# Optimization experiments

Hardware: AMD Instinct MI355X
Metric: run time of the kernel (lower is better)

## Reference

```python
import jax, jax.numpy as jnp
import numpy as np

D_MODEL, D_K, D_V = 1024, 64, 128
NUM_HEAD = D_MODEL // D_V  # 8


def setup_inputs() -> dict:
    key = jax.random.key(0)
    ks = jax.random.split(key, 6)
    B, SQ, SKV = 4, 2048, 2048
    return {
        "encoder_output": jax.random.normal(ks[0], (B, SKV, D_MODEL), jnp.float32),
        "pre_output": jax.random.normal(ks[1], (B, SQ, D_MODEL), jnp.float32),
        "Wq": jax.random.normal(ks[2], (D_MODEL, D_K * NUM_HEAD), jnp.float32) * 0.02,
        "Wk": jax.random.normal(ks[3], (D_MODEL, D_K * NUM_HEAD), jnp.float32) * 0.02,
        "Wv": jax.random.normal(ks[4], (D_MODEL, D_MODEL), jnp.float32) * 0.02,
        "Wo": jax.random.normal(ks[5], (D_MODEL, D_MODEL), jnp.float32) * 0.02,
    }


def reference(encoder_output, pre_output, Wq, Wk, Wv, Wo):
    B, SQ, _ = pre_output.shape
    SKV = encoder_output.shape[1]
    # projections (Linear, bias=False)
    q = pre_output @ Wq          # [B, SQ, H*d_k]
    k = encoder_output @ Wk      # [B, SKV, H*d_k]
    v = encoder_output @ Wv      # [B, SKV, H*d_v] (= d_model)
    # per-head contiguous slices == reshape into head dim
    q = q.reshape(B, SQ, NUM_HEAD, D_K)
    k = k.reshape(B, SKV, NUM_HEAD, D_K)
    v = v.reshape(B, SKV, NUM_HEAD, D_V)
    scale = 1.0 / np.sqrt(D_K).astype(np.float32)
    scores = jnp.einsum("bqhd,bkhd->bhqk", q, k) * scale  # [B,H,SQ,SKV]
    attn = jax.nn.softmax(scores, axis=-1)
    out = jnp.einsum("bhqk,bkhd->bqhd", attn, v)           # [B,SQ,H,d_v]
    out = out.reshape(B, SQ, NUM_HEAD * D_V)               # concat heads
    return out @ Wo
```

## Files before the change

kernel.cpp:

```cpp
#include <hip/hip_runtime.h>
#include <math.h>

#define D_MODEL 1024
#define DK 64
#define DV 128
#define NH 8
#define BB 4
#define SQL 2048
#define SKV 2048

typedef __bf16 bf16x8 __attribute__((ext_vector_type(8)));
typedef float f32x4 __attribute__((ext_vector_type(4)));

#if __has_builtin(__builtin_amdgcn_exp2f)
#define EXP2(x) __builtin_amdgcn_exp2f(x)
#else
#define EXP2(x) exp2f(x)
#endif

__device__ __forceinline__ ushort f2bf(float f) {
  unsigned u = __float_as_uint(f);
  u += 0x7FFFu + ((u >> 16) & 1u);
  return (ushort)(u >> 16);
}

#define GLDS16(g, l)                                                       \
  __builtin_amdgcn_global_load_lds(                                        \
      (const __attribute__((address_space(1))) unsigned int*)(g),          \
      (__attribute__((address_space(3))) unsigned int*)(l), 16, 0, 0)

__global__ __launch_bounds__(256) void cvt2_kernel(
    const float* __restrict__ s0, const float* __restrict__ s1,
    ushort* __restrict__ d0, ushort* __restrict__ d1, int n4) {
  const float* src = blockIdx.z ? s1 : s0;
  ushort* dst = blockIdx.z ? d1 : d0;
  int i = blockIdx.x * 256 + threadIdx.x;
  if (i >= n4) return;
  float4 v = ((const float4*)src)[i];
  ushort4 o;
  o.x = f2bf(v.x); o.y = f2bf(v.y); o.z = f2bf(v.z); o.w = f2bf(v.w);
  ((ushort4*)dst)[i] = o;
}

__global__ __launch_bounds__(256) void cvt_t4_kernel(
    const float* __restrict__ W0, const float* __restrict__ W1,
    const float* __restrict__ W2, const float* __restrict__ W3,
    ushort* __restrict__ T0, ushort* __restrict__ T1, ushort* __restrict__ T2,
    ushort* __restrict__ T3) {
  __shared__ ushort T[32][34];
  const int z = blockIdx.z;
  const int C = (z < 2) ? 512 : 1024;
  const int c0 = blockIdx.y * 32;
  if (c0 >= C) return;
  const float* W = (z == 0) ? W0 : (z == 1) ? W1 : (z == 2) ? W2 : W3;
  ushort* Wt = (z == 0) ? T0 : (z == 1) ? T1 : (z == 2) ? T2 : T3;
  const int R = 1024;
  const int r0 = blockIdx.x * 32;
  const int tx = threadIdx.x, ty = threadIdx.y;
#pragma unroll
  for (int i = 0; i < 4; ++i) {
    const int rr = ty + i * 8;
    T[rr][tx] = f2bf(W[(size_t)(r0 + rr) * C + c0 + tx]);
  }
  __syncthreads();
#pragma unroll
  for (int i = 0; i < 4; ++i) {
    const int rr = ty + i * 8;
    Wt[(size_t)(c0 + rr) * R + r0 + tx] = T[tx][rr];
  }
}

__global__ __launch_bounds__(256) void vtrans_kernel(
    const ushort* __restrict__ vb, ushort* __restrict__ vt) {
  __shared__ ushort T[32][34];
  const int s0 = blockIdx.x * 32;
  const int d0 = blockIdx.y * 32;
  const int bh = blockIdx.z;
  const int b = bh >> 3, h = bh & 7;
  const int tx = threadIdx.x, ty = threadIdx.y;
#pragma unroll
  for (int i = 0; i < 4; ++i) {
    const int rr = ty + i * 8;
    T[rr][tx] = vb[(size_t)(b * SKV + s0 + rr) * (NH * DV) + h * DV + d0 + tx];
  }
  __syncthreads();
#pragma unroll
  for (int i = 0; i < 4; ++i) {
    const int rr = ty + i * 8;
    vt[(size_t)bh * DV * SKV + (size_t)(d0 + rr) * SKV + s0 + tx] = T[tx][rr];
  }
}

template <typename OUT>
__device__ __forceinline__ void gemm_tile_core(ushort (*As)[32],
                                               ushort (*Bs)[32],
                                               const ushort* At,
                                               const ushort* Bt, OUT* Ct,
                                               int ldc, float osc, int K) {
  const int t = threadIdx.x;
  const int w = t >> 6, lane = t & 63;
  const int wm = (w >> 1) * 64, wn = (w & 1) * 64;
  const int lr = lane & 15, quad = lane >> 4;

  const int r0 = t >> 2;
  const int lb = (t & 3) ^ ((r0 >> 1) & 3);
  const ushort* gA0 = At + (size_t)r0 * K + lb * 8;
  const ushort* gA1 = At + (size_t)(r0 + 64) * K + lb * 8;
  const ushort* gB0 = Bt + (size_t)r0 * K + lb * 8;
  const ushort* gB1 = Bt + (size_t)(r0 + 64) * K + lb * 8;
  ushort* dA0 = (ushort*)As + t * 8;
  ushort* dA1 = (ushort*)As + t * 8 + 2048;
  ushort* dB0 = (ushort*)Bs + t * 8;
  ushort* dB1 = (ushort*)Bs + t * 8 + 2048;

  const int sw = (quad ^ ((lr >> 1) & 3)) * 8;

  f32x4 acc[4][4];
#pragma unroll
  for (int i = 0; i < 4; ++i)
#pragma unroll
    for (int j = 0; j < 4; ++j) acc[i][j] = (f32x4){0.f, 0.f, 0.f, 0.f};

  for (int k0 = 0; k0 < K; k0 += 32) {
    __syncthreads();
    GLDS16(gA0 + k0, dA0);
    GLDS16(gA1 + k0, dA1);
    GLDS16(gB0 + k0, dB0);
    GLDS16(gB1 + k0, dB1);
    __syncthreads();
    bf16x8 fa[4], fb[4];
#pragma unroll
    for (int i = 0; i < 4; ++i) fa[i] = *(const bf16x8*)&As[wm + i * 16 + lr][sw];
#pragma unroll
    for (int j = 0; j < 4; ++j) fb[j] = *(const bf16x8*)&Bs[wn + j * 16 + lr][sw];
#pragma unroll
    for (int i = 0; i < 4; ++i)
#pragma unroll
      for (int j = 0; j < 4; ++j)
        acc[i][j] = __builtin_amdgcn_mfma_f32_16x16x32_bf16(fa[i], fb[j],
                                                            acc[i][j], 0, 0, 0);
  }

#pragma unroll
  for (int i = 0; i < 4; ++i)
#pragma unroll
    for (int j = 0; j < 4; ++j)
#pragma unroll
      for (int r = 0; r < 4; ++r) {
        const int row = wm + i * 16 + quad * 4 + r;
        const int col = wn + j * 16 + lr;
        const float val = acc[i][j][r] * osc;
        if constexpr (sizeof(OUT) == 4)
          ((float*)Ct)[(size_t)row * ldc + col] = val;
        else
          ((ushort*)Ct)[(size_t)row * ldc + col] = f2bf(val);
      }
}

__global__ __launch_bounds__(256) void gemm_qkv_kernel(
    const ushort* __restrict__ preb, const ushort* __restrict__ encb,
    const ushort* __restrict__ WqkvT, ushort* __restrict__ qb,
    ushort* __restrict__ kb, ushort* __restrict__ vb, float qsc) {
  __shared__ ushort As[128][32];
  __shared__ ushort Bs[128][32];
  const int n0 = blockIdx.x * 128, m0 = blockIdx.y * 128;
  const int K = D_MODEL;
  const ushort* A;
  ushort* C;
  int ldc, ncol;
  float osc = 1.f;
  if (n0 < 512) {
    A = preb; C = qb; ldc = 512; ncol = n0; osc = qsc;
  } else if (n0 < 1024) {
    A = encb; C = kb; ldc = 512; ncol = n0 - 512;
  } else {
    A = encb; C = vb; ldc = 1024; ncol = n0 - 1024;
  }
  gemm_tile_core<ushort>(As, Bs, A + (size_t)m0 * K, WqkvT + (size_t)n0 * K,
                         C + (size_t)m0 * ldc + ncol, ldc, osc, K);
}

__global__ __launch_bounds__(256) void gemm_o_kernel(
    const ushort* __restrict__ ao, const ushort* __restrict__ WoT,
    float* __restrict__ out) {
  __shared__ ushort As[128][32];
  __shared__ ushort Bs[128][32];
  const int n0 = blockIdx.x * 128, m0 = blockIdx.y * 128;
  const int K = D_MODEL;
  gemm_tile_core<float>(As, Bs, ao + (size_t)m0 * K, WoT + (size_t)n0 * K,
                        out + (size_t)m0 * D_MODEL + n0, D_MODEL, 1.f, K);
}

__global__ __launch_bounds__(256) void attn_mfma_kernel(
    const ushort* __restrict__ Q, const ushort* __restrict__ Kb,
    const ushort* __restrict__ Vt, ushort* __restrict__ Oo) {
  __shared__ ushort Ks[64][64];
  __shared__ ushort Vs[128][64];
  __shared__ ushort Ps[4][32][68];

  const int t = threadIdx.x;
  const int qt = blockIdx.x, h = blockIdx.y, b = blockIdx.z;
  const int w = t >> 6, lane = t & 63;
  const int lr = lane & 15, quad = lane >> 4;
  const int q0 = qt * 128 + w * 32;

  union { bf16x8 v; ushort u[8]; } one8;
#pragma unroll
  for (int i = 0; i < 8; ++i) one8.u[i] = 0x3F80;

  bf16x8 aq[2][2];
#pragma unroll
  for (int mt = 0; mt < 2; ++mt)
#pragma unroll
    for (int kh = 0; kh < 2; ++kh)
      aq[mt][kh] = *(const bf16x8*)&Q[(size_t)(b * SQL + q0 + mt * 16 + lr) *
                                          (NH * DK) +
                                      h * DK + kh * 32 + quad * 8];

  f32x4 accO[2][9];
#pragma unroll
  for (int mt = 0; mt < 2; ++mt)
#pragma unroll
    for (int dn = 0; dn < 9; ++dn) accO[mt][dn] = (f32x4){0.f, 0.f, 0.f, 0.f};

  const ushort* kbase = Kb + (size_t)b * SKV * (NH * DK) + h * DK;
  const ushort* vbase = Vt + (size_t)(b * NH + h) * DV * SKV;

  const int srow = t >> 3;
  const int slb = (t & 7) ^ (srow & 7);
  const ushort* gK0 = kbase + (size_t)srow * (NH * DK) + slb * 8;
  const ushort* gK1 = kbase + (size_t)(srow + 32) * (NH * DK) + slb * 8;
  ushort* dK0 = (ushort*)Ks + t * 8;
  ushort* dK1 = (ushort*)Ks + t * 8 + 2048;
  const ushort* gV[4];
  ushort* dV[4];
#pragma unroll
  for (int it = 0; it < 4; ++it) {
    gV[it] = vbase + (size_t)(srow + 32 * it) * SKV + slb * 8;
    dV[it] = (ushort*)Vs + t * 8 + 2048 * it;
  }

  const int sw8 = lr & 7;

  for (int kv0 = 0; kv0 < SKV; kv0 += 64) {
    __syncthreads();
    GLDS16(gK0 + (size_t)kv0 * (NH * DK), dK0);
    GLDS16(gK1 + (size_t)kv0 * (NH * DK), dK1);
#pragma unroll
    for (int it = 0; it < 4; ++it) GLDS16(gV[it] + kv0, dV[it]);
    __syncthreads();

#pragma unroll
    for (int nt = 0; nt < 4; ++nt) {
      const bf16x8 fk0 = *(const bf16x8*)&Ks[nt * 16 + lr][(quad ^ sw8) * 8];
      const bf16x8 fk1 =
          *(const bf16x8*)&Ks[nt * 16 + lr][((4 + quad) ^ sw8) * 8];
#pragma unroll
      for (int mt = 0; mt < 2; ++mt) {
        f32x4 s = (f32x4){0.f, 0.f, 0.f, 0.f};
        s = __builtin_amdgcn_mfma_f32_16x16x32_bf16(fk0, aq[mt][0], s, 0, 0, 0);
        s = __builtin_amdgcn_mfma_f32_16x16x32_bf16(fk1, aq[mt][1], s, 0, 0, 0);
        const unsigned u0 = __float_as_uint(EXP2(s[0]));
        const unsigned u1 = __float_as_uint(EXP2(s[1]));
        const unsigned u2 = __float_as_uint(EXP2(s[2]));
        const unsigned u3 = __float_as_uint(EXP2(s[3]));
        uint2 dd;
        dd.x = __builtin_amdgcn_perm(u1, u0, 0x07060302u);
        dd.y = __builtin_amdgcn_perm(u3, u2, 0x07060302u);
        *(uint2*)&Ps[w][mt * 16 + lr][nt * 16 + quad * 4] = dd;
      }
    }

    bf16x8 ap[2][2];
#pragma unroll
    for (int mt = 0; mt < 2; ++mt)
#pragma unroll
      for (int kh = 0; kh < 2; ++kh) {
        union { bf16x8 v; uint2 u[2]; } fr;
        fr.u[0] = *(const uint2*)&Ps[w][mt * 16 + lr][kh * 32 + quad * 8];
        fr.u[1] = *(const uint2*)&Ps[w][mt * 16 + lr][kh * 32 + quad * 8 + 4];
        ap[mt][kh] = fr.v;
      }

#pragma unroll
    for (int dn = 0; dn < 8; ++dn) {
      const bf16x8 fv0 = *(const bf16x8*)&Vs[dn * 16 + lr][(quad ^ sw8) * 8];
      const bf16x8 fv1 =
          *(const bf16x8*)&Vs[dn * 16 + lr][((4 + quad) ^ sw8) * 8];
#pragma unroll
      for (int mt = 0; mt < 2; ++mt) {
        accO[mt][dn] = __builtin_amdgcn_mfma_f32_16x16x32_bf16(
            ap[mt][0], fv0, accO[mt][dn], 0, 0, 0);
        accO[mt][dn] = __builtin_amdgcn_mfma_f32_16x16x32_bf16(
            ap[mt][1], fv1, accO[mt][dn], 0, 0, 0);
      }
    }
#pragma unroll
    for (int mt = 0; mt < 2; ++mt) {
      accO[mt][8] = __builtin_amdgcn_mfma_f32_16x16x32_bf16(
          ap[mt][0], one8.v, accO[mt][8], 0, 0, 0);
      accO[mt][8] = __builtin_amdgcn_mfma_f32_16x16x32_bf16(
          ap[mt][1], one8.v, accO[mt][8], 0, 0, 0);
    }
  }

#pragma unroll
  for (int mt = 0; mt < 2; ++mt) {
    float inv[4];
#pragma unroll
    for (int r = 0; r < 4; ++r) inv[r] = 1.f / accO[mt][8][r];
#pragma unroll
    for (int dn = 0; dn < 8; ++dn)
#pragma unroll
      for (int r = 0; r < 4; ++r) {
        const size_t row = (size_t)b * SQL + q0 + mt * 16 + quad * 4 + r;
        Oo[row * D_MODEL + h * DV + dn * 16 + lr] =
            f2bf(accO[mt][dn][r] * inv[r]);
      }
  }
}

extern "C" void kernel_launch(void* const* d_in, const int* in_sizes, int n_in,
                              void* d_out, int out_size, void* d_ws,
                              size_t ws_size, hipStream_t stream) {
  const float* enc = (const float*)d_in[0];
  const float* pre = (const float*)d_in[1];
  const float* Wq = (const float*)d_in[2];
  const float* Wk = (const float*)d_in[3];
  const float* Wv = (const float*)d_in[4];
  const float* Wo = (const float*)d_in[5];
  float* out = (float*)d_out;

  const int M = BB * SQL;

  ushort* encb = (ushort*)d_ws;
  ushort* preb = encb + (size_t)M * D_MODEL;
  ushort* WqT = preb + (size_t)M * D_MODEL;
  ushort* WkT = WqT + (size_t)(NH * DK) * D_MODEL;
  ushort* WvT = WkT + (size_t)(NH * DK) * D_MODEL;
  ushort* WoT = WvT + (size_t)D_MODEL * D_MODEL;
  ushort* qb = WoT + (size_t)D_MODEL * D_MODEL;
  ushort* kb = qb + (size_t)M * (NH * DK);
  ushort* vt = kb + (size_t)M * (NH * DK);
  ushort* vb = vt + (size_t)M * D_MODEL;
  ushort* ao = encb;

  const int n4 = M * D_MODEL / 4;
  dim3 blk(256);
  dim3 tblk(32, 8);

  cvt2_kernel<<<dim3(n4 / 256, 1, 2), blk, 0, stream>>>(enc, pre, encb, preb,
                                                        n4);
  cvt_t4_kernel<<<dim3(32, 32, 4), tblk, 0, stream>>>(Wq, Wk, Wv, Wo, WqT, WkT,
                                                      WvT, WoT);

  gemm_qkv_kernel<<<dim3(16, 64), blk, 0, stream>>>(
      preb, encb, WqT, qb, kb, vb, 0.18033688011112042f);

  vtrans_kernel<<<dim3(SKV / 32, DV / 32, BB * NH), tblk, 0, stream>>>(vb, vt);

  attn_mfma_kernel<<<dim3(SQL / 128, NH, BB), blk, 0, stream>>>(qb, kb, vt, ao);

  gemm_o_kernel<<<dim3(8, 64), blk, 0, stream>>>(ao, WoT, out);
}
```

Baseline: 284.4 us.

## Fuse V transpose into QKV GEMM epilogue and widen attention KV tile

The QKV GEMM now writes the V projection straight into the transposed per-head layout by staging each tile through shared memory, so the separate vtrans kernel and its round trip through global memory are gone. The attention kernel now loads 128 KV rows per iteration instead of 64, with a new XOR swizzle on the V tile. It processes them in 32-wide chunks with a smaller P buffer, halving the number of barriers per KV sweep. The larger shared-memory footprint, about 52KB per block, may lower occupancy in the attention kernel.

After: 283.1 us. Within noise of the previous version (-0.5%).

```diff
diff --git a/kernel.cpp b/kernel.cpp
--- a/kernel.cpp
+++ b/kernel.cpp
@@ -18,10 +18,19 @@
 #define EXP2(x) exp2f(x)
 #endif
 
+#define MFMA16(a, b, c) __builtin_amdgcn_mfma_f32_16x16x32_bf16(a, b, c, 0, 0, 0)
+
 __device__ __forceinline__ ushort f2bf(float f) {
   unsigned u = __float_as_uint(f);
   u += 0x7FFFu + ((u >> 16) & 1u);
   return (ushort)(u >> 16);
+}
+__device__ __forceinline__ unsigned pk2bf(float lo, float hi) {
+  unsigned ul = __float_as_uint(lo);
+  unsigned uh = __float_as_uint(hi);
+  ul += 0x7FFFu + ((ul >> 16) & 1u);
+  uh += 0x7FFFu + ((uh >> 16) & 1u);
+  return __builtin_amdgcn_perm(uh, ul, 0x07060302u);
 }
 
 #define GLDS16(g, l)                                                       \
@@ -70,33 +79,11 @@
   }
 }
 
-__global__ __launch_bounds__(256) void vtrans_kernel(
-    const ushort* __restrict__ vb, ushort* __restrict__ vt) {
-  __shared__ ushort T[32][34];
-  const int s0 = blockIdx.x * 32;
-  const int d0 = blockIdx.y * 32;
-  const int bh = blockIdx.z;
-  const int b = bh >> 3, h = bh & 7;
-  const int tx = threadIdx.x, ty = threadIdx.y;
-#pragma unroll
-  for (int i = 0; i < 4; ++i) {
-    const int rr = ty + i * 8;
-    T[rr][tx] = vb[(size_t)(b * SKV + s0 + rr) * (NH * DV) + h * DV + d0 + tx];
-  }
-  __syncthreads();
-#pragma unroll
-  for (int i = 0; i < 4; ++i) {
-    const int rr = ty + i * 8;
-    vt[(size_t)bh * DV * SKV + (size_t)(d0 + rr) * SKV + s0 + tx] = T[tx][rr];
-  }
-}
-
-template <typename OUT>
-__device__ __forceinline__ void gemm_tile_core(ushort (*As)[32],
-                                               ushort (*Bs)[32],
-                                               const ushort* At,
-                                               const ushort* Bt, OUT* Ct,
-                                               int ldc, float osc, int K) {
+__device__ __forceinline__ void gemm_core_acc(ushort (*As)[32],
+                                              ushort (*Bs)[32],
+                                              const ushort* At,
+                                              const ushort* Bt, int K,
+                                              f32x4 (&acc)[4][4]) {
   const int t = threadIdx.x;
   const int w = t >> 6, lane = t & 63;
   const int wm = (w >> 1) * 64, wn = (w & 1) * 64;
@@ -115,7 +102,6 @@
 
   const int sw = (quad ^ ((lr >> 1) & 3)) * 8;
 
-  f32x4 acc[4][4];
 #pragma unroll
   for (int i = 0; i < 4; ++i)
 #pragma unroll
@@ -136,48 +122,67 @@
 #pragma unroll
     for (int i = 0; i < 4; ++i)
 #pragma unroll
-      for (int j = 0; j < 4; ++j)
-        acc[i][j] = __builtin_amdgcn_mfma_f32_16x16x32_bf16(fa[i], fb[j],
-                                                            acc[i][j], 0, 0, 0);
-  }
-
-#pragma unroll
-  for (int i = 0; i < 4; ++i)
-#pragma unroll
-    for (int j = 0; j < 4; ++j)
-#pragma unroll
-      for (int r = 0; r < 4; ++r) {
-        const int row = wm + i * 16 + quad * 4 + r;
-        const int col = wn + j * 16 + lr;
-        const float val = acc[i][j][r] * osc;
-        if constexpr (sizeof(OUT) == 4)
-          ((float*)Ct)[(size_t)row * ldc + col] = val;
-        else
-          ((ushort*)Ct)[(size_t)row * ldc + col] = f2bf(val);
-      }
+      for (int j = 0; j < 4; ++j) acc[i][j] = MFMA16(fa[i], fb[j], acc[i][j]);
+  }
 }
 
 __global__ __launch_bounds__(256) void gemm_qkv_kernel(
     const ushort* __restrict__ preb, const ushort* __restrict__ encb,
     const ushort* __restrict__ WqkvT, ushort* __restrict__ qb,
-    ushort* __restrict__ kb, ushort* __restrict__ vb, float qsc) {
-  __shared__ ushort As[128][32];
-  __shared__ ushort Bs[128][32];
+    ushort* __restrict__ kb, ushort* __restrict__ vt, float qsc) {
+  __shared__ ushort shm[17408];
+  ushort(*As)[32] = (ushort(*)[32])shm;
+  ushort(*Bs)[32] = (ushort(*)[32])(shm + 4096);
+
   const int n0 = blockIdx.x * 128, m0 = blockIdx.y * 128;
-  const int K = D_MODEL;
-  const ushort* A;
-  ushort* C;
-  int ldc, ncol;
-  float osc = 1.f;
-  if (n0 < 512) {
-    A = preb; C = qb; ldc = 512; ncol = n0; osc = qsc;
-  } else if (n0 < 1024) {
-    A = encb; C = kb; ldc = 512; ncol = n0 - 512;
+  const int t = threadIdx.x;
+  const int w = t >> 6, lane = t & 63;
+  const int wm = (w >> 1) * 64, wn = (w & 1) * 64;
+  const int lr = lane & 15, quad = lane >> 4;
+
+  const ushort* A = (n0 < 512) ? preb : encb;
+  f32x4 acc[4][4];
+  gemm_core_acc(As, Bs, A + (size_t)m0 * D_MODEL, WqkvT + (size_t)n0 * D_MODEL,
+                D_MODEL, acc);
+
+  if (n0 < 1024) {
+    ushort* C = (n0 < 512) ? qb : kb;
+    const int ncol = (n0 < 512) ? n0 : n0 - 512;
+    const float osc = (n0 < 512) ? qsc : 1.f;
+#pragma unroll
+    for (int i = 0; i < 4; ++i)
+#pragma unroll
+      for (int j = 0; j < 4; ++j)
+#pragma unroll
+        for (int r = 0; r < 4; ++r) {
+          const int row = m0 + wm + i * 16 + quad * 4 + r;
+          const int col = ncol + wn + j * 16 + lr;
+          C[(size_t)row * 512 + col] = f2bf(acc[i][j][r] * osc);
+        }
   } else {
-    A = encb; C = vb; ldc = 1024; ncol = n0 - 1024;
-  }
-  gemm_tile_core<ushort>(As, Bs, A + (size_t)m0 * K, WqkvT + (size_t)n0 * K,
-                         C + (size_t)m0 * ldc + ncol, ldc, osc, K);
+    const int h = (n0 - 1024) >> 7;
+    const int b = m0 >> 11;
+    const int skv0 = m0 & 2047;
+    __syncthreads();
+    ushort(*Ep)[68] = (ushort(*)[68])(shm + w * 4352);
+#pragma unroll
+    for (int i = 0; i < 4; ++i)
+#pragma unroll
+      for (int j = 0; j < 4; ++j) {
+        uint2 dd;
+        dd.x = pk2bf(acc[i][j][0], acc[i][j][1]);
+        dd.y = pk2bf(acc[i][j][2], acc[i][j][3]);
+        *(uint2*)&Ep[j * 16 + lr][i * 16 + quad * 4] = dd;
+      }
+    ushort* vbase =
+        vt + ((size_t)(b * NH + h) * DV + wn) * SKV + skv0 + wm;
+#pragma unroll
+    for (int rep = 0; rep < 8; ++rep) {
+      const int dvl = (lane >> 3) + rep * 8;
+      const int skvc = (lane & 7) * 8;
+      *(uint4*)&vbase[(size_t)dvl * SKV + skvc] = *(const uint4*)&Ep[dvl][skvc];
+    }
+  }
 }
 
 __global__ __launch_bounds__(256) void gemm_o_kernel(
@@ -186,17 +191,31 @@
   __shared__ ushort As[128][32];
   __shared__ ushort Bs[128][32];
   const int n0 = blockIdx.x * 128, m0 = blockIdx.y * 128;
-  const int K = D_MODEL;
-  gemm_tile_core<float>(As, Bs, ao + (size_t)m0 * K, WoT + (size_t)n0 * K,
-                        out + (size_t)m0 * D_MODEL + n0, D_MODEL, 1.f, K);
+  const int t = threadIdx.x;
+  const int w = t >> 6, lane = t & 63;
+  const int wm = (w >> 1) * 64, wn = (w & 1) * 64;
+  const int lr = lane & 15, quad = lane >> 4;
+  f32x4 acc[4][4];
+  gemm_core_acc(As, Bs, ao + (size_t)m0 * D_MODEL, WoT + (size_t)n0 * D_MODEL,
+                D_MODEL, acc);
+#pragma unroll
+  for (int i = 0; i < 4; ++i)
+#pragma unroll
+    for (int j = 0; j < 4; ++j)
+#pragma unroll
+      for (int r = 0; r < 4; ++r) {
+        const int row = m0 + wm + i * 16 + quad * 4 + r;
+        const int col = n0 + wn + j * 16 + lr;
+        out[(size_t)row * D_MODEL + col] = acc[i][j][r];
+      }
 }
 
 __global__ __launch_bounds__(256) void attn_mfma_kernel(
     const ushort* __restrict__ Q, const ushort* __restrict__ Kb,
     const ushort* __restrict__ Vt, ushort* __restrict__ Oo) {
-  __shared__ ushort Ks[64][64];
-  __shared__ ushort Vs[128][64];
-  __shared__ ushort Ps[4][32][68];
+  __shared__ ushort Ks[128][64];
+  __shared__ ushort Vs[128][128];
+  __shared__ ushort Ps[4][32][36];
 
   const int t = threadIdx.x;
   const int qt = blockIdx.x, h = blockIdx.y, b = blockIdx.z;
@@ -226,81 +245,67 @@
   const ushort* kbase = Kb + (size_t)b * SKV * (NH * DK) + h * DK;
   const ushort* vbase = Vt + (size_t)(b * NH + h) * DV * SKV;
 
-  const int srow = t >> 3;
-  const int slb = (t & 7) ^ (srow & 7);
-  const ushort* gK0 = kbase + (size_t)srow * (NH * DK) + slb * 8;
-  const ushort* gK1 = kbase + (size_t)(srow + 32) * (NH * DK) + slb * 8;
-  ushort* dK0 = (ushort*)Ks + t * 8;
-  ushort* dK1 = (ushort*)Ks + t * 8 + 2048;
-  const ushort* gV[4];
-  ushort* dV[4];
-#pragma unroll
-  for (int it = 0; it < 4; ++it) {
-    gV[it] = vbase + (size_t)(srow + 32 * it) * SKV + slb * 8;
-    dV[it] = (ushort*)Vs + t * 8 + 2048 * it;
-  }
-
-  const int sw8 = lr & 7;
-
-  for (int kv0 = 0; kv0 < SKV; kv0 += 64) {
-    __syncthreads();
-    GLDS16(gK0 + (size_t)kv0 * (NH * DK), dK0);
-    GLDS16(gK1 + (size_t)kv0 * (NH * DK), dK1);
-#pragma unroll
-    for (int it = 0; it < 4; ++it) GLDS16(gV[it] + kv0, dV[it]);
-    __syncthreads();
-
-#pragma unroll
-    for (int nt = 0; nt < 4; ++nt) {
-      const bf16x8 fk0 = *(const bf16x8*)&Ks[nt * 16 + lr][(quad ^ sw8) * 8];
-      const bf16x8 fk1 =
-          *(const bf16x8*)&Ks[nt * 16 + lr][((4 + quad) ^ sw8) * 8];
+  const int krow = t >> 3;
+  const int kblk = (t & 7) ^ (krow & 7);
+  const ushort* gK = kbase + (size_t)krow * (NH * DK) + kblk * 8;
+  ushort* dK = (ushort*)Ks + t * 8;
+  const int vrow = t >> 4;
+  const int vkv = ((t & 15) ^ (vrow & 15)) * 8;
+  const ushort* gV = vbase + (size_t)vrow * SKV + vkv;
+  ushort* dV = (ushort*)Vs + t * 8;
+
+  const int swk = lr & 7;
+
+  for (int kv0 = 0; kv0 < SKV; kv0 += 128) {
+    __syncthreads();
+#pragma unroll
+    for (int rd = 0; rd < 4; ++rd)
+      GLDS16(gK + (size_t)(kv0 + rd * 32) * (NH * DK), dK + rd * 2048);
+#pragma unroll
+    for (int rd = 0; rd < 8; ++rd)
+      GLDS16(gV + (size_t)rd * 16 * SKV + kv0, dV + rd * 2048);
+    __syncthreads();
+
+#pragma unroll
+    for (int c = 0; c < 4; ++c) {
+#pragma unroll
+      for (int tt = 0; tt < 2; ++tt) {
+        const int nt = c * 2 + tt;
+        const bf16x8 fk0 = *(const bf16x8*)&Ks[nt * 16 + lr][(quad ^ swk) * 8];
+        const bf16x8 fk1 =
+            *(const bf16x8*)&Ks[nt * 16 + lr][((4 + quad) ^ swk) * 8];
+#pragma unroll
+        for (int mt = 0; mt < 2; ++mt) {
+          f32x4 s = (f32x4){0.f, 0.f, 0.f, 0.f};
+          s = MFMA16(fk0, aq[mt][0], s);
+          s = MFMA16(fk1, aq[mt][1], s);
+          const unsigned u0 = __float_as_uint(EXP2(s[0]));
+          const unsigned u1 = __float_as_uint(EXP2(s[1]));
+          const unsigned u2 = __float_as_uint(EXP2(s[2]));
+          const unsigned u3 = __float_as_uint(EXP2(s[3]));
+          uint2 dd;
+          dd.x = __builtin_amdgcn_perm(u1, u0, 0x07060302u);
+          dd.y = __builtin_amdgcn_perm(u3, u2, 0x07060302u);
+          *(uint2*)&Ps[w][mt * 16 + lr][tt * 16 + quad * 4] = dd;
+        }
+      }
+      bf16x8 ap[2];
 #pragma unroll
       for (int mt = 0; mt < 2; ++mt) {
-        f32x4 s = (f32x4){0.f, 0.f, 0.f, 0.f};
-        s = __builtin_amdgcn_mfma_f32_16x16x32_bf16(fk0, aq[mt][0], s, 0, 0, 0);
-        s = __builtin_amdgcn_mfma_f32_16x16x32_bf16(fk1, aq[mt][1], s, 0, 0, 0);
-        const unsigned u0 = __float_as_uint(EXP2(s[0]));
-        const unsigned u1 = __float_as_uint(EXP2(s[1]));
-        const unsigned u2 = __float_as_uint(EXP2(s[2]));
-        const unsigned u3 = __float_as_uint(EXP2(s[3]));
-        uint2 dd;
-        dd.x = __builtin_amdgcn_perm(u1, u0, 0x07060302u);
-        dd.y = __builtin_amdgcn_perm(u3, u2, 0x07060302u);
-        *(uint2*)&Ps[w][mt * 16 + lr][nt * 16 + quad * 4] = dd;
-      }
-    }
-
-    bf16x8 ap[2][2];
-#pragma unroll
-    for (int mt = 0; mt < 2; ++mt)
-#pragma unroll
-      for (int kh = 0; kh < 2; ++kh) {
         union { bf16x8 v; uint2 u[2]; } fr;
-        fr.u[0] = *(const uint2*)&Ps[w][mt * 16 + lr][kh * 32 + quad * 8];
-        fr.u[1] = *(const uint2*)&Ps[w][mt * 16 + lr][kh * 32 + quad * 8 + 4];
-        ap[mt][kh] = fr.v;
-      }
-
-#pragma unroll
-    for (int dn = 0; dn < 8; ++dn) {
-      const bf16x8 fv0 = *(const bf16x8*)&Vs[dn * 16 + lr][(quad ^ sw8) * 8];
-      const bf16x8 fv1 =
-          *(const bf16x8*)&Vs[dn * 16 + lr][((4 + quad) ^ sw8) * 8];
-#pragma unroll
-      for (int mt = 0; mt < 2; ++mt) {
-        accO[mt][dn] = __builtin_amdgcn_mfma_f32_16x16x32_bf16(
-            ap[mt][0], fv0, accO[mt][dn], 0, 0, 0);
-        accO[mt][dn] = __builtin_amdgcn_mfma_f32_16x16x32_bf16(
-            ap[mt][1], fv1, accO[mt][dn], 0, 0, 0);
-      }
-    }
-#pragma unroll
-    for (int mt = 0; mt < 2; ++mt) {
-      accO[mt][8] = __builtin_amdgcn_mfma_f32_16x16x32_bf16(
-          ap[mt][0], one8.v, accO[mt][8], 0, 0, 0);
-      accO[mt][8] = __builtin_amdgcn_mfma_f32_16x16x32_bf16(
-          ap[mt][1], one8.v, accO[mt][8], 0, 0, 0);
+        fr.u[0] = *(const uint2*)&Ps[w][mt * 16 + lr][quad * 8];
+        fr.u[1] = *(const uint2*)&Ps[w][mt * 16 + lr][quad * 8 + 4];
+        ap[mt] = fr.v;
+      }
+#pragma unroll
+      for (int dn = 0; dn < 8; ++dn) {
+        const bf16x8 fv =
+            *(const bf16x8*)&Vs[dn * 16 + lr][((c * 4 + quad) ^ lr) * 8];
+        accO[0][dn] = MFMA16(ap[0], fv, accO[0][dn]);
+        accO[1][dn] = MFMA16(ap[1], fv, accO[1][dn]);
+      }
+      accO[0][8] = MFMA16(ap[0], one8.v, accO[0][8]);
+      accO[1][8] = MFMA16(ap[1], one8.v, accO[1][8]);
     }
   }
 
@@ -342,7 +347,6 @@
   ushort* qb = WoT + (size_t)D_MODEL * D_MODEL;
   ushort* kb = qb + (size_t)M * (NH * DK);
   ushort* vt = kb + (size_t)M * (NH * DK);
-  ushort* vb = vt + (size_t)M * D_MODEL;
   ushort* ao = encb;
 
   const int n4 = M * D_MODEL / 4;
@@ -355,9 +359,7 @@
                                                       WvT, WoT);
 
   gemm_qkv_kernel<<<dim3(16, 64), blk, 0, stream>>>(
-      preb, encb, WqT, qb, kb, vb, 0.18033688011112042f);
-
-  vtrans_kernel<<<dim3(SKV / 32, DV / 32, BB * NH), tblk, 0, stream>>>(vb, vt);
+      preb, encb, WqT, qb, kb, vt, 0.18033688011112042f);
 
   attn_mfma_kernel<<<dim3(SQL / 128, NH, BB), blk, 0, stream>>>(qb, kb, vt, ao);
 
```
